# Performance work log

Hardware: AMD Instinct MI355X
Metric: run time of the kernel (lower is better)

The kernel has to match this reference:

```python
import jax, jax.numpy as jnp
import numpy as np

N_BASIS = 20
R_MAX = 3.5

# e3nn normalize2mom constant for silu: 1/sqrt(E[silu(z)^2]), z~N(0,1) (analytic quadrature)
_trapz = getattr(np, "trapezoid", np.trapz)
_z = np.linspace(-12.0, 12.0, 100001)
_phi = np.exp(-0.5 * _z**2) / np.sqrt(2.0 * np.pi)
_silu = _z / (1.0 + np.exp(-_z))
SILU_CST = float(1.0 / np.sqrt(_trapz(_silu**2 * _phi, _z)))  # ~1.679


def norm_silu(x):
    return SILU_CST * jax.nn.silu(x)


def spherical_harmonics_lmax3(pos):
    # component-normalized real spherical harmonics up to l=3, e3nn axis convention (y up)
    u = pos / jnp.linalg.norm(pos, axis=-1, keepdims=True)
    x, y, z = u[..., 0], u[..., 1], u[..., 2]
    x2, y2, z2 = x * x, y * y, z * z
    s3, s5, s15 = jnp.sqrt(3.0), jnp.sqrt(5.0), jnp.sqrt(15.0)
    s7, s105 = jnp.sqrt(7.0), jnp.sqrt(105.0)
    s35_8, s21_8 = jnp.sqrt(35.0 / 8.0), jnp.sqrt(21.0 / 8.0)
    sh = [
        jnp.ones_like(x),                                                   # l=0
        s3 * x, s3 * y, s3 * z,                                             # l=1
        s15 * x * z, s15 * x * y, s5 * (y2 - 0.5 * (x2 + z2)),
        s15 * y * z, 0.5 * s15 * (z2 - x2),                                 # l=2
        s35_8 * x * (3.0 * z2 - x2), s105 * x * y * z,
        s21_8 * x * (5.0 * y2 - 1.0), 0.5 * s7 * y * (5.0 * y2 - 3.0),
        s21_8 * z * (5.0 * y2 - 1.0), 0.5 * s105 * y * (z2 - x2),
        s35_8 * z * (z2 - 3.0 * x2),                                        # l=3
    ]
    return jnp.stack(sh, axis=-1)  # [E, 16]


def soft_one_hot_gaussian(d):
    # e3nn soft_one_hot_linspace(start=0, end=3.5, number=20, basis='gaussian', cutoff=True)
    values = jnp.linspace(0.0, R_MAX, N_BASIS + 2)[1:-1]
    step = R_MAX / (N_BASIS + 1)
    diff = (d[:, None] - values[None, :]) / step
    return jnp.exp(-diff * diff) / 1.12


def setup_inputs() -> dict:
    E, N = 2_000_000, 125_000
    key = jax.random.key(0)
    k = jax.random.split(key, 6)
    return {
        "pos": jax.random.normal(k[0], (E, 3), jnp.float32),
        "x_right": jax.random.normal(k[1], (E, 1), jnp.float32),
        "x_left": jax.random.normal(k[2], (N, 1), jnp.float32),
        "W1": jax.random.normal(k[3], (20, 30), jnp.float32),
        "W2": jax.random.normal(k[4], (30, 5), jnp.float32),
        "origin_index": jax.random.randint(k[5], (E,), 0, N),
    }


def reference(pos, x_right, x_left, W1, W2, origin_index):
    sh = spherical_harmonics_lmax3(pos)                 # [E, 16], component norm
    d = jnp.linalg.norm(pos, axis=-1)                   # [E]
    emb = soft_one_hot_gaussian(d)                      # [E, 20]
    # e3nn FullyConnectedNet([20, 30, 5], silu): x @ W / sqrt(fan_in), normalized act on hidden
    h = norm_silu(emb @ (W1 / jnp.sqrt(jnp.asarray(W1.shape[0], jnp.float32))))
    tp_weights = h @ (W2 / jnp.sqrt(jnp.asarray(W2.shape[0], jnp.float32)))  # [E, 5]
    # tp1: FullyConnectedTensorProduct('1x0e', sh, '5x0e'): only CG path is 0e(x)0e->0e
    # (single path -> path-normalization factor 1; Y_0 = 1 under component normalization)
    h_right = tp_weights * x_right * sh[:, :1]          # [E, 5]
    # tp2: FullTensorProduct('1x0e', '5x0e') -> '5x0e': plain scalar product per channel
    product = x_left[origin_index] * h_right            # [E, 5]
    return jnp.sum(product)
```

## Files before the change

### kernel.cpp

```cpp
#include <hip/hip_runtime.h>
#include <hip/hip_bf16.h>


#define TN 8192
#define DMAX 5.0f
#define NBLK 2048

__device__ __constant__ float kSiluCst = 1.6765581f;

__global__ __launch_bounds__(256) void build_lut_kernel(
    const float* __restrict__ W1, const float* __restrict__ W2,
    float* __restrict__ table)
{
    int t = blockIdx.x * 256 + threadIdx.x;
    int entry = t >> 5;
    int k = t & 31;
    int kk = (k < 30) ? k : 29;

    float d  = (float)entry * (DMAX / (float)TN);
    float t6 = 6.0f * d;
    const float w1scale = 1.0f / (1.12f * sqrtf(20.0f));

    float a = 0.0f;
    #pragma unroll
    for (int j = 0; j < 20; ++j) {
        float df = t6 - (float)(j + 1);
        float e  = __expf(-df * df);
        a = fmaf(e * w1scale, W1[j * 30 + kk], a);
    }
    float s = a / (1.0f + __expf(-a));

    float w2s = 0.0f;
    #pragma unroll
    for (int c = 0; c < 5; ++c) w2s += W2[kk * 5 + c];

    float contrib = (k < 30) ? s * w2s * (kSiluCst / sqrtf(30.0f)) : 0.0f;

    #pragma unroll
    for (int m = 16; m > 0; m >>= 1) contrib += __shfl_xor(contrib, m, 32);

    if (k == 0 && entry < TN) table[entry] = contrib;
}

__global__ __launch_bounds__(256) void edge_sum_kernel(
    const float* __restrict__ pos, const float* __restrict__ xr,
    const float* __restrict__ xl, const int* __restrict__ oi,
    const float* __restrict__ table, double* __restrict__ partials, int E)
{
    __shared__ float lut[TN];
    __shared__ double swv[4];

    {
        const float4* t4 = (const float4*)table;
        float4* l4 = (float4*)lut;
        for (int i = threadIdx.x; i < TN / 4; i += 256) l4[i] = t4[i];
    }
    __syncthreads();

    const float scale = (float)TN / DMAX;
    double acc = 0.0;
    int stride = gridDim.x * blockDim.x;
    for (int e = blockIdx.x * blockDim.x + threadIdx.x; e < E; e += stride) {
        float px = pos[3 * e + 0];
        float py = pos[3 * e + 1];
        float pz = pos[3 * e + 2];
        float d  = sqrtf(fmaf(px, px, fmaf(py, py, pz * pz)));
        float u  = fminf(d * scale, (float)(TN - 1) - 1e-3f);
        int   i0 = (int)u;
        float fr = u - (float)i0;
        float f0 = lut[i0];
        float f1 = lut[i0 + 1];
        float f  = fmaf(fr, f1 - f0, f0);
        float v  = f * xr[e] * xl[oi[e]];
        acc += (double)v;
    }

    #pragma unroll
    for (int off = 32; off > 0; off >>= 1) acc += __shfl_down(acc, off);
    int lane = threadIdx.x & 63, wv = threadIdx.x >> 6;
    if (lane == 0) swv[wv] = acc;
    __syncthreads();
    if (threadIdx.x == 0)
        partials[blockIdx.x] = (swv[0] + swv[1]) + (swv[2] + swv[3]);
}

__global__ __launch_bounds__(256) void final_reduce_kernel(
    const double* __restrict__ partials, int n, float* __restrict__ out)
{
    __shared__ double sm[256];
    double a = 0.0;
    for (int i = threadIdx.x; i < n; i += 256) a += partials[i];
    sm[threadIdx.x] = a;
    __syncthreads();
    #pragma unroll
    for (int s = 128; s > 0; s >>= 1) {
        if (threadIdx.x < (unsigned)s) sm[threadIdx.x] += sm[threadIdx.x + s];
        __syncthreads();
    }
    if (threadIdx.x == 0) out[0] = (float)sm[0];
}

extern "C" void kernel_launch(void* const* d_in, const int* in_sizes, int n_in,
                              void* d_out, int out_size, void* d_ws, size_t ws_size,
                              hipStream_t stream) {
    const float* pos = (const float*)d_in[0];
    const float* xr  = (const float*)d_in[1];
    const float* xl  = (const float*)d_in[2];
    const float* W1  = (const float*)d_in[3];
    const float* W2  = (const float*)d_in[4];
    const int*   oi  = (const int*)d_in[5];
    float* out = (float*)d_out;

    int E = in_sizes[1];

    float*  table    = (float*)d_ws;
    double* partials = (double*)((char*)d_ws + (size_t)TN * sizeof(float));

    hipLaunchKernelGGL(build_lut_kernel, dim3((TN * 32) / 256), dim3(256), 0, stream,
                       W1, W2, table);
    hipLaunchKernelGGL(edge_sum_kernel, dim3(NBLK), dim3(256), 0, stream,
                       pos, xr, xl, oi, table, partials, E);
    hipLaunchKernelGGL(final_reduce_kernel, dim3(1), dim3(256), 0, stream,
                       partials, NBLK, out);
}
```

Measured before the change: 28.85 us.

## Vectorize edge loads, shrink LUT, and fuse final reduction via last-block counter

The edge kernel now handles 8 contiguous edges per thread with float4/int4 loads for pos, x_right and indices, and gathers x_left values up front to expose memory-level parallelism. The LUT drops from 8192 to 2048 entries, which cuts the build work and the per-block shared-memory fill. The separate final reduce kernel is replaced by a threadfence plus atomic counter, so the last block to finish sums the partials, saving a launch. The fixed grid of 1024 blocks × 256 × 8 edges covers exactly 2M edges, which ties the grid to this problem size, and the coarser LUT reduces interpolation accuracy.

Result: slower. 55.01 us (+90.7%).

```diff
diff --git a/kernel.cpp b/kernel.cpp
--- a/kernel.cpp
+++ b/kernel.cpp
@@ -1,23 +1,26 @@
 #include <hip/hip_runtime.h>
-#include <hip/hip_bf16.h>
 
 
-#define TN 8192
-#define DMAX 5.0f
-#define NBLK 2048
+#define TN   2048
+#define DMAXF 5.0f
+#define NBLK 1024
+#define TPB  256
+#define EPT  8
 
 __device__ __constant__ float kSiluCst = 1.6765581f;
 
 __global__ __launch_bounds__(256) void build_lut_kernel(
     const float* __restrict__ W1, const float* __restrict__ W2,
-    float* __restrict__ table)
+    float* __restrict__ table, unsigned* __restrict__ counter)
 {
+    if (blockIdx.x == 0 && threadIdx.x == 0) *counter = 0u;
+
     int t = blockIdx.x * 256 + threadIdx.x;
     int entry = t >> 5;
     int k = t & 31;
     int kk = (k < 30) ? k : 29;
 
-    float d  = (float)entry * (DMAX / (float)TN);
+    float d  = (float)entry * (DMAXF / (float)TN);
     float t6 = 6.0f * d;
     const float w1scale = 1.0f / (1.12f * sqrtf(20.0f));
 
@@ -42,37 +45,75 @@
     if (k == 0 && entry < TN) table[entry] = contrib;
 }
 
-__global__ __launch_bounds__(256) void edge_sum_kernel(
+__global__ __launch_bounds__(TPB) void edge_sum_kernel(
     const float* __restrict__ pos, const float* __restrict__ xr,
     const float* __restrict__ xl, const int* __restrict__ oi,
-    const float* __restrict__ table, double* __restrict__ partials, int E)
+    const float* __restrict__ table, double* __restrict__ partials,
+    unsigned* __restrict__ counter, float* __restrict__ out, int E)
 {
     __shared__ float lut[TN];
-    __shared__ double swv[4];
+    __shared__ double swv[TPB / 64];
+    __shared__ double sm[TPB];
+    __shared__ int slast;
 
     {
         const float4* t4 = (const float4*)table;
         float4* l4 = (float4*)lut;
-        for (int i = threadIdx.x; i < TN / 4; i += 256) l4[i] = t4[i];
+        l4[threadIdx.x]       = t4[threadIdx.x];
+        l4[threadIdx.x + TPB] = t4[threadIdx.x + TPB];
     }
     __syncthreads();
 
-    const float scale = (float)TN / DMAX;
+    const float scale = (float)TN / DMAXF;
+    const float umax  = (float)(TN - 1) - 1e-3f;
+
+    int  gtid = blockIdx.x * TPB + threadIdx.x;
+    long base = (long)gtid * EPT;
     double acc = 0.0;
-    int stride = gridDim.x * blockDim.x;
-    for (int e = blockIdx.x * blockDim.x + threadIdx.x; e < E; e += stride) {
-        float px = pos[3 * e + 0];
-        float py = pos[3 * e + 1];
-        float pz = pos[3 * e + 2];
-        float d  = sqrtf(fmaf(px, px, fmaf(py, py, pz * pz)));
-        float u  = fminf(d * scale, (float)(TN - 1) - 1e-3f);
-        int   i0 = (int)u;
-        float fr = u - (float)i0;
-        float f0 = lut[i0];
-        float f1 = lut[i0 + 1];
-        float f  = fmaf(fr, f1 - f0, f0);
-        float v  = f * xr[e] * xl[oi[e]];
-        acc += (double)v;
+
+    if (base + EPT <= (long)E) {
+        float p[EPT * 3]; float xrv[EPT]; int oiv[EPT];
+        const float4* p4 = (const float4*)(pos + base * 3);
+        float4 t;
+        t = p4[0]; p[0]  = t.x; p[1]  = t.y; p[2]  = t.z; p[3]  = t.w;
+        t = p4[1]; p[4]  = t.x; p[5]  = t.y; p[6]  = t.z; p[7]  = t.w;
+        t = p4[2]; p[8]  = t.x; p[9]  = t.y; p[10] = t.z; p[11] = t.w;
+        t = p4[3]; p[12] = t.x; p[13] = t.y; p[14] = t.z; p[15] = t.w;
+        t = p4[4]; p[16] = t.x; p[17] = t.y; p[18] = t.z; p[19] = t.w;
+        t = p4[5]; p[20] = t.x; p[21] = t.y; p[22] = t.z; p[23] = t.w;
+        const float4* x4 = (const float4*)(xr + base);
+        t = x4[0]; xrv[0] = t.x; xrv[1] = t.y; xrv[2] = t.z; xrv[3] = t.w;
+        t = x4[1]; xrv[4] = t.x; xrv[5] = t.y; xrv[6] = t.z; xrv[7] = t.w;
+        const int4* o4 = (const int4*)(oi + base);
+        int4 ti;
+        ti = o4[0]; oiv[0] = ti.x; oiv[1] = ti.y; oiv[2] = ti.z; oiv[3] = ti.w;
+        ti = o4[1]; oiv[4] = ti.x; oiv[5] = ti.y; oiv[6] = ti.z; oiv[7] = ti.w;
+
+        float xlv[EPT];
+        #pragma unroll
+        for (int j = 0; j < EPT; ++j) xlv[j] = xl[oiv[j]];
+
+        #pragma unroll
+        for (int j = 0; j < EPT; ++j) {
+            float x = p[3 * j], y = p[3 * j + 1], z = p[3 * j + 2];
+            float d  = sqrtf(fmaf(x, x, fmaf(y, y, z * z)));
+            float u  = fminf(d * scale, umax);
+            int   i0 = (int)u;
+            float fr = u - (float)i0;
+            float f0 = lut[i0], f1 = lut[i0 + 1];
+            float f  = fmaf(fr, f1 - f0, f0);
+            acc += (double)(f * xrv[j] * xlv[j]);
+        }
+    } else if (base < (long)E) {
+        for (long e = base; e < (long)E; ++e) {
+            float x = pos[3 * e], y = pos[3 * e + 1], z = pos[3 * e + 2];
+            float d  = sqrtf(fmaf(x, x, fmaf(y, y, z * z)));
+            float u  = fminf(d * scale, umax);
+            int   i0 = (int)u;
+            float fr = u - (float)i0;
+            float f  = fmaf(fr, lut[i0 + 1] - lut[i0], lut[i0]);
+            acc += (double)(f * xr[e] * xl[oi[e]]);
+        }
     }
 
     #pragma unroll
@@ -80,24 +121,27 @@
     int lane = threadIdx.x & 63, wv = threadIdx.x >> 6;
     if (lane == 0) swv[wv] = acc;
     __syncthreads();
-    if (threadIdx.x == 0)
+    if (threadIdx.x == 0) {
         partials[blockIdx.x] = (swv[0] + swv[1]) + (swv[2] + swv[3]);
-}
+        __threadfence();
+        unsigned prev = atomicAdd(counter, 1u);
+        slast = (prev == (unsigned)(gridDim.x - 1)) ? 1 : 0;
+    }
+    __syncthreads();
 
-__global__ __launch_bounds__(256) void final_reduce_kernel(
-    const double* __restrict__ partials, int n, float* __restrict__ out)
-{
-    __shared__ double sm[256];
-    double a = 0.0;
-    for (int i = threadIdx.x; i < n; i += 256) a += partials[i];
-    sm[threadIdx.x] = a;
-    __syncthreads();
-    #pragma unroll
-    for (int s = 128; s > 0; s >>= 1) {
-        if (threadIdx.x < (unsigned)s) sm[threadIdx.x] += sm[threadIdx.x + s];
+    if (slast) {
+        __threadfence();
+        double a = 0.0;
+        for (int i = threadIdx.x; i < NBLK; i += TPB) a += partials[i];
+        sm[threadIdx.x] = a;
         __syncthreads();
+        #pragma unroll
+        for (int s = 128; s > 0; s >>= 1) {
+            if (threadIdx.x < (unsigned)s) sm[threadIdx.x] += sm[threadIdx.x + s];
+            __syncthreads();
+        }
+        if (threadIdx.x == 0) out[0] = (float)sm[0];
     }
-    if (threadIdx.x == 0) out[0] = (float)sm[0];
 }
 
 extern "C" void kernel_launch(void* const* d_in, const int* in_sizes, int n_in,
@@ -113,13 +157,13 @@
 
     int E = in_sizes[1];
 
-    float*  table    = (float*)d_ws;
-    double* partials = (double*)((char*)d_ws + (size_t)TN * sizeof(float));
+    float*    table    = (float*)d_ws;
+    double*   partials = (double*)((char*)d_ws + (size_t)TN * sizeof(float));
+    unsigned* counter  = (unsigned*)((char*)d_ws + (size_t)TN * sizeof(float)
+                                     + (size_t)NBLK * sizeof(double));
 
     hipLaunchKernelGGL(build_lut_kernel, dim3((TN * 32) / 256), dim3(256), 0, stream,
-                       W1, W2, table);
-    hipLaunchKernelGGL(edge_sum_kernel, dim3(NBLK), dim3(256), 0, stream,
-                       pos, xr, xl, oi, table, partials, E);
-    hipLaunchKernelGGL(final_reduce_kernel, dim3(1), dim3(256), 0, stream,
-                       partials, NBLK, out);
+                       W1, W2, table, counter);
+    hipLaunchKernelGGL(edge_sum_kernel, dim3(NBLK), dim3(TPB), 0, stream,
+                       pos, xr, xl, oi, table, partials, counter, out, E);
 }
```
